# Optimization experiments

Hardware: AMD Instinct MI355X
Metric: run time of the kernel (lower is better)

Reference implementation:

```python
import jax, jax.numpy as jnp
import numpy as np

N_NODES = 50000
N_EDGES = 800000
IN_CH = 128
H1, C1 = 2, 64            # gat1: heads=2, out=64 -> concat 128
H2, C2 = 1, 32            # gat2: heads=1, out=out_channels=32, concat=False
NEG_SLOPE = 0.2           # PyG GATConv default negative_slope


def setup_inputs() -> dict:
    key = jax.random.key(0)
    ks = jax.random.split(key, 12)
    s = 0.05
    return {
        "x": jax.random.normal(ks[0], (N_NODES, IN_CH), dtype=jnp.float32),
        "edge_index": jax.random.randint(ks[1], (2, N_EDGES), 0, N_NODES, dtype=jnp.int64),
        # layer 1 params
        "W1": jax.random.normal(ks[2], (IN_CH, H1 * C1), dtype=jnp.float32) * s,
        "a1_src": jax.random.normal(ks[3], (H1, C1), dtype=jnp.float32) * s,
        "a1_dst": jax.random.normal(ks[4], (H1, C1), dtype=jnp.float32) * s,
        "b1": jax.random.normal(ks[5], (H1 * C1,), dtype=jnp.float32) * s,
        # layer 2 params
        "W2": jax.random.normal(ks[6], (H1 * C1, H2 * C2), dtype=jnp.float32) * s,
        "a2_src": jax.random.normal(ks[7], (H2, C2), dtype=jnp.float32) * s,
        "a2_dst": jax.random.normal(ks[8], (H2, C2), dtype=jnp.float32) * s,
        "b2": jax.random.normal(ks[9], (C2,), dtype=jnp.float32) * s,
    }


def _gat_conv(x, src, dst, W, a_src, a_dst, b, heads, out_ch, concat):
    """PyG GATConv (eval mode, self-loops already in src/dst)."""
    n = x.shape[0]
    h = (x @ W).reshape(n, heads, out_ch)               # [N,H,C]
    s_src = jnp.sum(h * a_src, axis=-1)                  # [N,H]
    s_dst = jnp.sum(h * a_dst, axis=-1)                  # [N,H]
    e = jax.nn.leaky_relu(s_src[src] + s_dst[dst], NEG_SLOPE)   # [E,H]
    # segment softmax over incoming edges of each destination node
    emax = jax.ops.segment_max(e, dst, num_segments=n)   # [N,H]
    emax = jax.lax.stop_gradient(emax)
    ee = jnp.exp(e - emax[dst])
    den = jax.ops.segment_sum(ee, dst, num_segments=n)   # [N,H]
    alpha = ee / den[dst]                                # [E,H]
    out = jax.ops.segment_sum(h[src] * alpha[..., None], dst, num_segments=n)  # [N,H,C]
    out = out.reshape(n, heads * out_ch) if concat else out.mean(axis=1)
    return out + b


def reference(x, edge_index, W1, a1_src, a1_dst, b1, W2, a2_src, a2_dst, b2):
    n = x.shape[0]
    loops = jnp.arange(n, dtype=edge_index.dtype)
    src = jnp.concatenate([edge_index[0], loops])
    dst = jnp.concatenate([edge_index[1], loops])
    h = _gat_conv(x, src, dst, W1, a1_src, a1_dst, b1, H1, C1, concat=True)
    h = jax.nn.elu(h)
    out = _gat_conv(h, src, dst, W2, a2_src, a2_dst, b2, H2, C2, concat=False)
    return out
```

## Files before the change

### kernel.cpp

```cpp
#include <hip/hip_runtime.h>
#include <hip/hip_fp16.h>
#include <math.h>

#define N_NODES 50000
#define N_EDGES 800000
#define E_TOT   (N_EDGES + N_NODES)
#define SCAN_BLK 1024
#define SCAN_NB  ((N_NODES + SCAN_BLK - 1) / SCAN_BLK)

__global__ __launch_bounds__(256) void gemm1_tiled(
    const float* __restrict__ x, const float* __restrict__ W,
    const float* __restrict__ a_src, const float* __restrict__ a_dst,
    __half* __restrict__ h, float* __restrict__ s_src, float* __restrict__ s_dst)
{
    __shared__ float xs[128][68];
    __shared__ float wt[64][68];
    const int tid  = threadIdx.x;
    const int colT = tid & 15;
    const int rowT = tid >> 4;
    const int half = blockIdx.x & 1;
    const int r0   = (blockIdx.x >> 1) * 128;
    const int c0   = half * 64;

    float acc[4][8];
    #pragma unroll
    for (int j = 0; j < 4; ++j)
        #pragma unroll
        for (int i = 0; i < 8; ++i) acc[j][i] = 0.f;

    for (int kc = 0; kc < 2; ++kc) {
        const int kbase = kc * 64;
        #pragma unroll
        for (int it = 0; it < 8; ++it) {
            int q = it * 256 + tid;
            int row = q >> 4, k4 = q & 15;
            float4 v = make_float4(0.f, 0.f, 0.f, 0.f);
            if (r0 + row < N_NODES)
                v = *(const float4*)&x[(size_t)(r0 + row) * 128 + kbase + k4 * 4];
            *(float4*)&xs[row][k4 * 4] = v;
        }
        #pragma unroll
        for (int it = 0; it < 4; ++it) {
            int q = it * 256 + tid;
            int c = q & 63, k4 = q >> 6;
            float4 v;
            v.x = W[(kbase + k4 * 4 + 0) * 128 + c0 + c];
            v.y = W[(kbase + k4 * 4 + 1) * 128 + c0 + c];
            v.z = W[(kbase + k4 * 4 + 2) * 128 + c0 + c];
            v.w = W[(kbase + k4 * 4 + 3) * 128 + c0 + c];
            *(float4*)&wt[c][k4 * 4] = v;
        }
        __syncthreads();
        #pragma unroll 4
        for (int k4 = 0; k4 < 16; ++k4) {
            float4 wv[4], xv[8];
            #pragma unroll
            for (int j = 0; j < 4; ++j) wv[j] = *(const float4*)&wt[colT + 16 * j][k4 * 4];
            #pragma unroll
            for (int i = 0; i < 8; ++i) xv[i] = *(const float4*)&xs[rowT + 16 * i][k4 * 4];
            #pragma unroll
            for (int j = 0; j < 4; ++j)
                #pragma unroll
                for (int i = 0; i < 8; ++i)
                    acc[j][i] += wv[j].x * xv[i].x + wv[j].y * xv[i].y
                               + wv[j].z * xv[i].z + wv[j].w * xv[i].w;
        }
        __syncthreads();
    }

    #pragma unroll
    for (int i = 0; i < 8; ++i) {
        const int row = r0 + rowT + 16 * i;
        float vs = 0.f, vd = 0.f;
        #pragma unroll
        for (int j = 0; j < 4; ++j) {
            const int c = c0 + colT + 16 * j;
            const float a = acc[j][i];
            vs += a * a_src[c];
            vd += a * a_dst[c];
            if (row < N_NODES) h[(size_t)row * 128 + c] = __float2half(a);
        }
        #pragma unroll
        for (int off = 8; off >= 1; off >>= 1) {
            vs += __shfl_xor(vs, off, 64);
            vd += __shfl_xor(vd, off, 64);
        }
        if (colT == 0 && row < N_NODES) {
            s_src[row * 2 + half] = vs;
            s_dst[row * 2 + half] = vd;
        }
    }
}

__global__ __launch_bounds__(256) void gemm2_tiled(
    const float* __restrict__ h2, const float* __restrict__ W,
    const float* __restrict__ a_src, const float* __restrict__ a_dst,
    __half* __restrict__ g, float* __restrict__ s_src, float* __restrict__ s_dst)
{
    __shared__ float xs[128][68];
    __shared__ float wt[32][68];
    const int tid  = threadIdx.x;
    const int colT = tid & 7;
    const int rowT = tid >> 3;
    const int r0   = blockIdx.x * 128;

    float acc[4][4];
    #pragma unroll
    for (int j = 0; j < 4; ++j)
        #pragma unroll
        for (int i = 0; i < 4; ++i) acc[j][i] = 0.f;

    for (int kc = 0; kc < 2; ++kc) {
        const int kbase = kc * 64;
        #pragma unroll
        for (int it = 0; it < 8; ++it) {
            int q = it * 256 + tid;
            int row = q >> 4, k4 = q & 15;
            float4 v = make_float4(0.f, 0.f, 0.f, 0.f);
            if (r0 + row < N_NODES)
                v = *(const float4*)&h2[(size_t)(r0 + row) * 128 + kbase + k4 * 4];
            *(float4*)&xs[row][k4 * 4] = v;
        }
        #pragma unroll
        for (int it = 0; it < 2; ++it) {
            int q = it * 256 + tid;
            int c = q & 31, k4 = q >> 5;
            float4 v;
            v.x = W[(kbase + k4 * 4 + 0) * 32 + c];
            v.y = W[(kbase + k4 * 4 + 1) * 32 + c];
            v.z = W[(kbase + k4 * 4 + 2) * 32 + c];
            v.w = W[(kbase + k4 * 4 + 3) * 32 + c];
            *(float4*)&wt[c][k4 * 4] = v;
        }
        __syncthreads();
        #pragma unroll 4
        for (int k4 = 0; k4 < 16; ++k4) {
            float4 wv[4], xv[4];
            #pragma unroll
            for (int j = 0; j < 4; ++j) wv[j] = *(const float4*)&wt[colT + 8 * j][k4 * 4];
            #pragma unroll
            for (int i = 0; i < 4; ++i) xv[i] = *(const float4*)&xs[rowT + 32 * i][k4 * 4];
            #pragma unroll
            for (int j = 0; j < 4; ++j)
                #pragma unroll
                for (int i = 0; i < 4; ++i)
                    acc[j][i] += wv[j].x * xv[i].x + wv[j].y * xv[i].y
                               + wv[j].z * xv[i].z + wv[j].w * xv[i].w;
        }
        __syncthreads();
    }

    #pragma unroll
    for (int i = 0; i < 4; ++i) {
        const int row = r0 + rowT + 32 * i;
        float vs = 0.f, vd = 0.f;
        #pragma unroll
        for (int j = 0; j < 4; ++j) {
            const int c = colT + 8 * j;
            const float a = acc[j][i];
            vs += a * a_src[c];
            vd += a * a_dst[c];
            if (row < N_NODES) g[(size_t)row * 32 + c] = __float2half(a);
        }
        #pragma unroll
        for (int off = 4; off >= 1; off >>= 1) {
            vs += __shfl_xor(vs, off, 64);
            vd += __shfl_xor(vd, off, 64);
        }
        if (colT == 0 && row < N_NODES) {
            s_src[row] = vs;
            s_dst[row] = vd;
        }
    }
}

__global__ void hist_kernel(const int* __restrict__ edst, int* __restrict__ deg)
{
    int e = blockIdx.x * blockDim.x + threadIdx.x;
    if (e >= E_TOT) return;
    int d = (e < N_EDGES) ? edst[e] : (e - N_EDGES);
    atomicAdd(&deg[d], 1);
}

__global__ __launch_bounds__(1024) void scanA_kernel(
    const int* __restrict__ deg, int* __restrict__ locscan, int* __restrict__ partial)
{
    __shared__ int buf[SCAN_BLK];
    const int t = threadIdx.x;
    const int i = blockIdx.x * SCAN_BLK + t;
    int v = (i < N_NODES) ? deg[i] : 0;
    buf[t] = v;
    __syncthreads();
    #pragma unroll
    for (int off = 1; off < SCAN_BLK; off <<= 1) {
        int xx = (t >= off) ? buf[t - off] : 0;
        __syncthreads();
        buf[t] += xx;
        __syncthreads();
    }
    if (i < N_NODES) locscan[i] = buf[t] - v;
    if (t == SCAN_BLK - 1) partial[blockIdx.x] = buf[t];
}

__global__ void scanB_kernel(int* __restrict__ partial)
{
    const int t = threadIdx.x;
    int orig = (t < SCAN_NB) ? partial[t] : 0;
    int v = orig;
    #pragma unroll
    for (int off = 1; off < 64; off <<= 1) {
        int xx = __shfl_up(v, off, 64);
        if (t >= off) v += xx;
    }
    if (t < SCAN_NB) partial[t] = v - orig;
}

__global__ void scanC_kernel(const int* __restrict__ locscan, const int* __restrict__ partial,
                             int* __restrict__ offsets, int* __restrict__ cursor)
{
    int i = blockIdx.x * 256 + threadIdx.x;
    if (i >= N_NODES) return;
    int o = locscan[i] + partial[i >> 10];
    offsets[i] = o;
    cursor[i]  = o;
    if (i == 0) offsets[N_NODES] = E_TOT;
}

__global__ void scatter_kernel(const int* __restrict__ esrc, const int* __restrict__ edst,
                               int* __restrict__ cursor, int* __restrict__ csr_src)
{
    int e = blockIdx.x * blockDim.x + threadIdx.x;
    if (e >= E_TOT) return;
    int s, d;
    if (e < N_EDGES) { s = esrc[e]; d = edst[e]; } else { s = d = e - N_EDGES; }
    int pos = atomicAdd(&cursor[d], 1);
    csr_src[pos] = s;
}

__global__ __launch_bounds__(256) void fused_agg1_kernel(
    const int* __restrict__ csr_src, const int* __restrict__ offsets,
    const float* __restrict__ s_src, const float* __restrict__ s_dst,
    const __half* __restrict__ h, const float* __restrict__ b,
    float* __restrict__ h2)
{
    const int wid  = threadIdx.x >> 6;
    const int lane = threadIdx.x & 63;
    const int p    = lane & 15;
    const int slot = lane >> 4;
    const bool headhi = p >= 8;
    const int d = blockIdx.x * 4 + wid;
    if (d >= N_NODES) return;
    const int beg = offsets[d], end = offsets[d + 1];
    const float sd0 = s_dst[d * 2], sd1 = s_dst[d * 2 + 1];
    float m0 = -1e30f, m1 = -1e30f;
    float den0 = 0.f, den1 = 0.f;
    float acc[8];
    #pragma unroll
    for (int k = 0; k < 8; ++k) acc[k] = 0.f;

    for (int pos = beg; pos < end; pos += 64) {
        const int n = min(64, end - pos);
        int s = 0;
        float v0 = -1e30f, v1 = -1e30f;
        if (lane < n) {
            s = csr_src[pos + lane];
            const float2 ss = *(const float2*)&s_src[s * 2];
            v0 = ss.x + sd0;  v0 = v0 > 0.f ? v0 : 0.2f * v0;
            v1 = ss.y + sd1;  v1 = v1 > 0.f ? v1 : 0.2f * v1;
        }
        float cm0 = v0, cm1 = v1;
        #pragma unroll
        for (int off = 32; off >= 1; off >>= 1) {
            cm0 = fmaxf(cm0, __shfl_xor(cm0, off, 64));
            cm1 = fmaxf(cm1, __shfl_xor(cm1, off, 64));
        }
        const float nm0 = fmaxf(m0, cm0), nm1 = fmaxf(m1, cm1);
        const float sc0 = __expf(m0 - nm0), sc1 = __expf(m1 - nm1);
        den0 *= sc0; den1 *= sc1;
        const float asc = headhi ? sc1 : sc0;
        #pragma unroll
        for (int k = 0; k < 8; ++k) acc[k] *= asc;
        m0 = nm0; m1 = nm1;
        const float e0 = (lane < n) ? __expf(v0 - nm0) : 0.f;
        const float e1 = (lane < n) ? __expf(v1 - nm1) : 0.f;
        float t0 = e0, t1 = e1;
        #pragma unroll
        for (int off = 32; off >= 1; off >>= 1) {
            t0 += __shfl_xor(t0, off, 64);
            t1 += __shfl_xor(t1, off, 64);
        }
        den0 += t0; den1 += t1;

        const int steps = (n + 3) >> 2;
        int j  = slot;
        int si = __shfl(s, j, 64);
        float4 raw = *(const float4*)&h[(size_t)si * 128 + p * 8];
        float av0 = __shfl(e0, j, 64);
        float av1 = __shfl(e1, j, 64);
        float av  = headhi ? av1 : av0;
        for (int i = 0; i < steps; ++i) {
            const float4 cur = raw;
            const float  ac  = av;
            if (i + 1 < steps) {
                j   = 4 * (i + 1) + slot;
                si  = __shfl(s, j, 64);
                raw = *(const float4*)&h[(size_t)si * 128 + p * 8];
                av0 = __shfl(e0, j, 64);
                av1 = __shfl(e1, j, 64);
                av  = headhi ? av1 : av0;
            }
            const __half2* hp = (const __half2*)&cur;
            #pragma unroll
            for (int k = 0; k < 4; ++k) {
                const float2 f = __half22float2(hp[k]);
                acc[2 * k]     += ac * f.x;
                acc[2 * k + 1] += ac * f.y;
            }
        }
    }
    #pragma unroll
    for (int k = 0; k < 8; ++k) {
        acc[k] += __shfl_xor(acc[k], 16, 64);
        acc[k] += __shfl_xor(acc[k], 32, 64);
    }
    if (slot == 0) {
        const float den = headhi ? den1 : den0;
        float o[8];
        #pragma unroll
        for (int k = 0; k < 8; ++k) {
            o[k] = acc[k] / den + b[p * 8 + k];
            o[k] = o[k] > 0.f ? o[k] : expm1f(o[k]);
        }
        *(float4*)&h2[(size_t)d * 128 + p * 8]     = make_float4(o[0], o[1], o[2], o[3]);
        *(float4*)&h2[(size_t)d * 128 + p * 8 + 4] = make_float4(o[4], o[5], o[6], o[7]);
    }
}

__global__ __launch_bounds__(256) void fused_agg2_kernel(
    const int* __restrict__ csr_src, const int* __restrict__ offsets,
    const float* __restrict__ s_src, const float* __restrict__ s_dst,
    const __half* __restrict__ g, const float* __restrict__ b,
    float* __restrict__ out)
{
    const int grp      = threadIdx.x >> 5;
    const int q        = threadIdx.x & 31;
    const int halfbase = threadIdx.x & 32;
    const int p2       = q & 3;
    const int slot2    = q >> 2;
    const int d = blockIdx.x * 8 + grp;
    if (d >= N_NODES) return;
    const int beg = offsets[d], end = offsets[d + 1];
    const float sd = s_dst[d];
    float m = -1e30f, den = 0.f;
    float acc[8];
    #pragma unroll
    for (int k = 0; k < 8; ++k) acc[k] = 0.f;

    for (int pos = beg; pos < end; pos += 32) {
        const int n = min(32, end - pos);
        int s = 0;
        float v = -1e30f;
        if (q < n) {
            s = csr_src[pos + q];
            v = s_src[s] + sd;  v = v > 0.f ? v : 0.2f * v;
        }
        float cm = v;
        #pragma unroll
        for (int off = 16; off >= 1; off >>= 1)
            cm = fmaxf(cm, __shfl_xor(cm, off, 32));
        const float nm = fmaxf(m, cm);
        const float sc = __expf(m - nm);
        den *= sc;
        #pragma unroll
        for (int k = 0; k < 8; ++k) acc[k] *= sc;
        m = nm;
        const float e = (q < n) ? __expf(v - nm) : 0.f;
        float t = e;
        #pragma unroll
        for (int off = 16; off >= 1; off >>= 1)
            t += __shfl_xor(t, off, 32);
        den += t;

        const int steps = (n + 7) >> 3;
        int j  = slot2;
        int si = __shfl(s, halfbase + j, 64);
        float4 raw = *(const float4*)&g[(size_t)si * 32 + p2 * 8];
        float av = __shfl(e, halfbase + j, 64);
        for (int i = 0; i < steps; ++i) {
            const float4 cur = raw;
            const float  ac  = av;
            if (i + 1 < steps) {
                j  = 8 * (i + 1) + slot2;
                si = __shfl(s, halfbase + j, 64);
                raw = *(const float4*)&g[(size_t)si * 32 + p2 * 8];
                av  = __shfl(e, halfbase + j, 64);
            }
            const __half2* gp = (const __half2*)&cur;
            #pragma unroll
            for (int k = 0; k < 4; ++k) {
                const float2 f = __half22float2(gp[k]);
                acc[2 * k]     += ac * f.x;
                acc[2 * k + 1] += ac * f.y;
            }
        }
    }
    #pragma unroll
    for (int k = 0; k < 8; ++k) {
        acc[k] += __shfl_xor(acc[k], 4, 32);
        acc[k] += __shfl_xor(acc[k], 8, 32);
        acc[k] += __shfl_xor(acc[k], 16, 32);
    }
    if (slot2 == 0) {
        float o[8];
        #pragma unroll
        for (int k = 0; k < 8; ++k)
            o[k] = acc[k] / den + b[p2 * 8 + k];
        *(float4*)&out[(size_t)d * 32 + p2 * 8]     = make_float4(o[0], o[1], o[2], o[3]);
        *(float4*)&out[(size_t)d * 32 + p2 * 8 + 4] = make_float4(o[4], o[5], o[6], o[7]);
    }
}

extern "C" void kernel_launch(void* const* d_in, const int* in_sizes, int n_in,
                              void* d_out, int out_size, void* d_ws, size_t ws_size,
                              hipStream_t stream)
{
    const float* x   = (const float*)d_in[0];
    const int*   ei  = (const int*)d_in[1];
    const float* W1  = (const float*)d_in[2];
    const float* a1s = (const float*)d_in[3];
    const float* a1d = (const float*)d_in[4];
    const float* b1  = (const float*)d_in[5];
    const float* W2  = (const float*)d_in[6];
    const float* a2s = (const float*)d_in[7];
    const float* a2d = (const float*)d_in[8];
    const float* b2  = (const float*)d_in[9];
    float* out = (float*)d_out;

    const int* esrc = ei;
    const int* edst = ei + N_EDGES;

    float* ws = (float*)d_ws;
    __half* h1 = (__half*)ws;
    float* h2  = ws  + (size_t)N_NODES * 128;
    float* s1s = h2  + (size_t)N_NODES * 128;
    float* s1d = s1s + 2 * N_NODES;
    float* s2s = s1d + 2 * N_NODES;
    float* s2d = s2s + N_NODES;
    int* deg     = (int*)(s2d + N_NODES);
    int* offsets = deg + N_NODES;
    int* cursor  = offsets + N_NODES + 1;
    int* csr_src = cursor + N_NODES;
    int* locscan = csr_src + E_TOT;
    int* partial = locscan + N_NODES;
    __half* g2 = (__half*)ws;

    hipMemsetAsync(deg, 0, (size_t)N_NODES * 4, stream);
    hist_kernel<<<(E_TOT + 255) / 256, 256, 0, stream>>>(edst, deg);
    scanA_kernel<<<SCAN_NB, SCAN_BLK, 0, stream>>>(deg, locscan, partial);
    scanB_kernel<<<1, 64, 0, stream>>>(partial);
    scanC_kernel<<<(N_NODES + 255) / 256, 256, 0, stream>>>(locscan, partial, offsets, cursor);
    scatter_kernel<<<(E_TOT + 255) / 256, 256, 0, stream>>>(esrc, edst, cursor, csr_src);

    gemm1_tiled<<<((N_NODES + 127) / 128) * 2, 256, 0, stream>>>(x, W1, a1s, a1d, h1, s1s, s1d);
    fused_agg1_kernel<<<(N_NODES + 3) / 4, 256, 0, stream>>>(
        csr_src, offsets, s1s, s1d, h1, b1, h2);

    gemm2_tiled<<<(N_NODES + 127) / 128, 256, 0, stream>>>(h2, W2, a2s, a2d, g2, s2s, s2d);
    fused_agg2_kernel<<<(N_NODES + 7) / 8, 256, 0, stream>>>(
        csr_src, offsets, s2s, s2d, g2, b2, out);
}
```

Measured before the change: 235.1 us.

## Drop online max in GAT softmax and broadcast edge records through LDS

Both aggregation kernels stop tracking a running maximum. They exponentiate the leaky-ReLU scores directly and keep per-lane partial denominators, which are reduced once after the edge loop. This removes the per-chunk max and sum shuffle reductions and the accumulator rescaling. Source index and attention weight are now staged in a per-wave shared-memory record array instead of being fetched with repeated __shfl calls. The trade-off is numerical: without max subtraction, exp can overflow if attention scores grow large, so correctness relies on scores staying moderate.

```diff
diff --git a/kernel.cpp b/kernel.cpp
--- a/kernel.cpp
+++ b/kernel.cpp
@@ -243,6 +243,7 @@
     const __half* __restrict__ h, const float* __restrict__ b,
     float* __restrict__ h2)
 {
+    __shared__ float4 rec[4][64];
     const int wid  = threadIdx.x >> 6;
     const int lane = threadIdx.x & 63;
     const int p    = lane & 15;
@@ -252,7 +253,6 @@
     if (d >= N_NODES) return;
     const int beg = offsets[d], end = offsets[d + 1];
     const float sd0 = s_dst[d * 2], sd1 = s_dst[d * 2 + 1];
-    float m0 = -1e30f, m1 = -1e30f;
     float den0 = 0.f, den1 = 0.f;
     float acc[8];
     #pragma unroll
@@ -261,53 +261,32 @@
     for (int pos = beg; pos < end; pos += 64) {
         const int n = min(64, end - pos);
         int s = 0;
-        float v0 = -1e30f, v1 = -1e30f;
+        float e0 = 0.f, e1 = 0.f;
         if (lane < n) {
             s = csr_src[pos + lane];
             const float2 ss = *(const float2*)&s_src[s * 2];
-            v0 = ss.x + sd0;  v0 = v0 > 0.f ? v0 : 0.2f * v0;
-            v1 = ss.y + sd1;  v1 = v1 > 0.f ? v1 : 0.2f * v1;
-        }
-        float cm0 = v0, cm1 = v1;
-        #pragma unroll
-        for (int off = 32; off >= 1; off >>= 1) {
-            cm0 = fmaxf(cm0, __shfl_xor(cm0, off, 64));
-            cm1 = fmaxf(cm1, __shfl_xor(cm1, off, 64));
-        }
-        const float nm0 = fmaxf(m0, cm0), nm1 = fmaxf(m1, cm1);
-        const float sc0 = __expf(m0 - nm0), sc1 = __expf(m1 - nm1);
-        den0 *= sc0; den1 *= sc1;
-        const float asc = headhi ? sc1 : sc0;
-        #pragma unroll
-        for (int k = 0; k < 8; ++k) acc[k] *= asc;
-        m0 = nm0; m1 = nm1;
-        const float e0 = (lane < n) ? __expf(v0 - nm0) : 0.f;
-        const float e1 = (lane < n) ? __expf(v1 - nm1) : 0.f;
-        float t0 = e0, t1 = e1;
-        #pragma unroll
-        for (int off = 32; off >= 1; off >>= 1) {
-            t0 += __shfl_xor(t0, off, 64);
-            t1 += __shfl_xor(t1, off, 64);
-        }
-        den0 += t0; den1 += t1;
+            float v0 = ss.x + sd0;  v0 = v0 > 0.f ? v0 : 0.2f * v0;
+            float v1 = ss.y + sd1;  v1 = v1 > 0.f ? v1 : 0.2f * v1;
+            e0 = __expf(v0);
+            e1 = __expf(v1);
+        }
+        den0 += e0;
+        den1 += e1;
+        rec[wid][lane] = make_float4(__int_as_float(s), e0, e1, 0.f);
 
         const int steps = (n + 3) >> 2;
-        int j  = slot;
-        int si = __shfl(s, j, 64);
-        float4 raw = *(const float4*)&h[(size_t)si * 128 + p * 8];
-        float av0 = __shfl(e0, j, 64);
-        float av1 = __shfl(e1, j, 64);
-        float av  = headhi ? av1 : av0;
+        float4 r  = rec[wid][slot];
+        int    si = __float_as_int(r.x);
+        float4 hv = *(const float4*)&h[(size_t)si * 128 + p * 8];
+        float  av = headhi ? r.z : r.y;
         for (int i = 0; i < steps; ++i) {
-            const float4 cur = raw;
+            const float4 cur = hv;
             const float  ac  = av;
             if (i + 1 < steps) {
-                j   = 4 * (i + 1) + slot;
-                si  = __shfl(s, j, 64);
-                raw = *(const float4*)&h[(size_t)si * 128 + p * 8];
-                av0 = __shfl(e0, j, 64);
-                av1 = __shfl(e1, j, 64);
-                av  = headhi ? av1 : av0;
+                r  = rec[wid][4 * (i + 1) + slot];
+                si = __float_as_int(r.x);
+                hv = *(const float4*)&h[(size_t)si * 128 + p * 8];
+                av = headhi ? r.z : r.y;
             }
             const __half2* hp = (const __half2*)&cur;
             #pragma unroll
@@ -319,6 +298,11 @@
         }
     }
     #pragma unroll
+    for (int off = 32; off >= 1; off >>= 1) {
+        den0 += __shfl_xor(den0, off, 64);
+        den1 += __shfl_xor(den1, off, 64);
+    }
+    #pragma unroll
     for (int k = 0; k < 8; ++k) {
         acc[k] += __shfl_xor(acc[k], 16, 64);
         acc[k] += __shfl_xor(acc[k], 32, 64);
@@ -342,16 +326,16 @@
     const __half* __restrict__ g, const float* __restrict__ b,
     float* __restrict__ out)
 {
-    const int grp      = threadIdx.x >> 5;
-    const int q        = threadIdx.x & 31;
-    const int halfbase = threadIdx.x & 32;
-    const int p2       = q & 3;
-    const int slot2    = q >> 2;
+    __shared__ float2 rec[8][32];
+    const int grp   = threadIdx.x >> 5;
+    const int q     = threadIdx.x & 31;
+    const int p2    = q & 3;
+    const int slot2 = q >> 2;
     const int d = blockIdx.x * 8 + grp;
     if (d >= N_NODES) return;
     const int beg = offsets[d], end = offsets[d + 1];
     const float sd = s_dst[d];
-    float m = -1e30f, den = 0.f;
+    float den = 0.f;
     float acc[8];
     #pragma unroll
     for (int k = 0; k < 8; ++k) acc[k] = 0.f;
@@ -359,41 +343,28 @@
     for (int pos = beg; pos < end; pos += 32) {
         const int n = min(32, end - pos);
         int s = 0;
-        float v = -1e30f;
+        float e = 0.f;
         if (q < n) {
             s = csr_src[pos + q];
-            v = s_src[s] + sd;  v = v > 0.f ? v : 0.2f * v;
-        }
-        float cm = v;
-        #pragma unroll
-        for (int off = 16; off >= 1; off >>= 1)
-            cm = fmaxf(cm, __shfl_xor(cm, off, 32));
-        const float nm = fmaxf(m, cm);
-        const float sc = __expf(m - nm);
-        den *= sc;
-        #pragma unroll
-        for (int k = 0; k < 8; ++k) acc[k] *= sc;
-        m = nm;
-        const float e = (q < n) ? __expf(v - nm) : 0.f;
-        float t = e;
-        #pragma unroll
-        for (int off = 16; off >= 1; off >>= 1)
-            t += __shfl_xor(t, off, 32);
-        den += t;
+            float v = s_src[s] + sd;  v = v > 0.f ? v : 0.2f * v;
+            e = __expf(v);
+        }
+        den += e;
+        rec[grp][q] = make_float2(__int_as_float(s), e);
 
         const int steps = (n + 7) >> 3;
-        int j  = slot2;
-        int si = __shfl(s, halfbase + j, 64);
-        float4 raw = *(const float4*)&g[(size_t)si * 32 + p2 * 8];
-        float av = __shfl(e, halfbase + j, 64);
+        float2 r  = rec[grp][slot2];
+        int    si = __float_as_int(r.x);
+        float4 gv = *(const float4*)&g[(size_t)si * 32 + p2 * 8];
+        float  av = r.y;
         for (int i = 0; i < steps; ++i) {
-            const float4 cur = raw;
+            const float4 cur = gv;
             const float  ac  = av;
             if (i + 1 < steps) {
-                j  = 8 * (i + 1) + slot2;
-                si = __shfl(s, halfbase + j, 64);
-                raw = *(const float4*)&g[(size_t)si * 32 + p2 * 8];
-                av  = __shfl(e, halfbase + j, 64);
+                r  = rec[grp][8 * (i + 1) + slot2];
+                si = __float_as_int(r.x);
+                gv = *(const float4*)&g[(size_t)si * 32 + p2 * 8];
+                av = r.y;
             }
             const __half2* gp = (const __half2*)&cur;
             #pragma unroll
@@ -404,6 +375,9 @@
             }
         }
     }
+    #pragma unroll
+    for (int off = 16; off >= 1; off >>= 1)
+        den += __shfl_xor(den, off, 32);
     #pragma unroll
     for (int k = 0; k < 8; ++k) {
         acc[k] += __shfl_xor(acc[k], 4, 32);
```

Result: slower. 246.0 us (+4.6%).
